# Kernel optimization log

Measured on AMD Instinct MI355X. Metric: run time of the kernel, lower is better.

## Reference

```python
import jax, jax.numpy as jnp
import numpy as np


def _grid_sample_bilinear_zeros(src, y, x):
    """Bilinear grid_sample, zeros padding, pixel-space coords.
    src: [B,C,H,W]; y,x: [B,H,W] float pixel coordinates (y along H, x along W).
    Returns [B,C,H,W].
    """
    B, C, H, W = src.shape
    y0 = jnp.floor(y)
    x0 = jnp.floor(x)
    y1 = y0 + 1.0
    x1 = x0 + 1.0
    wy1 = y - y0
    wy0 = 1.0 - wy1
    wx1 = x - x0
    wx0 = 1.0 - wx1

    b_idx = jnp.arange(B)[:, None, None]  # [B,1,1]

    def gather(yi, xi):
        valid = ((yi >= 0) & (yi < H) & (xi >= 0) & (xi < W)).astype(src.dtype)
        yc = jnp.clip(yi, 0, H - 1).astype(jnp.int32)
        xc = jnp.clip(xi, 0, W - 1).astype(jnp.int32)
        v = src[b_idx, :, yc, xc]  # advanced indexing -> [B,H,W,C]
        return v * valid[..., None]

    out = (gather(y0, x0) * (wy0 * wx0)[..., None]
           + gather(y0, x1) * (wy0 * wx1)[..., None]
           + gather(y1, x0) * (wy1 * wx0)[..., None]
           + gather(y1, x1) * (wy1 * wx1)[..., None])  # [B,H,W,C]
    return out.transpose(0, 3, 1, 2)


def setup_inputs() -> dict:
    key = jax.random.key(0)
    k1, k2 = jax.random.split(key)
    B, C, H, W = 8, 64, 256, 256
    src = jax.random.normal(k1, (B, C, H, W), dtype=jnp.float32)
    flow = jax.random.normal(k2, (B, 2, H, W), dtype=jnp.float32)
    return {"src": src, "flow": flow}


def reference(src, flow):
    B, C, H, W = src.shape
    # identity grid (meshgrid 'ij'): channel 0 = row index (H), channel 1 = col index (W)
    gy = jnp.arange(H, dtype=flow.dtype)[None, :, None]  # [1,H,1]
    gx = jnp.arange(W, dtype=flow.dtype)[None, None, :]  # [1,1,W]
    new_y = gy + flow[:, 0]  # [B,H,W]
    new_x = gx + flow[:, 1]
    # normalize to [-1,1] (as the module does) ...
    ny = 2.0 * (new_y / (H - 1) - 0.5)
    nx = 2.0 * (new_x / (W - 1) - 0.5)
    # ... then grid_sample with align_corners=True maps back to pixel space
    py = (ny + 1.0) * 0.5 * (H - 1)
    px = (nx + 1.0) * 0.5 * (W - 1)
    return _grid_sample_bilinear_zeros(src, py, px)
```

## Files before the change

### kernel.cpp

```cpp
#include <hip/hip_runtime.h>

#define B_ 8
#define C_ 64
#define H_ 256
#define W_ 256
#define RT 8
#define CG 8
#define WIN 32
#define PITCH 264

__global__ __launch_bounds__(256) void st_warp_kernel(
    const float* __restrict__ src,
    const float* __restrict__ flow,
    float* __restrict__ out)
{
    __shared__ float tile[WIN * PITCH];

    const int HW = H_ * W_;

    int id    = blockIdx.x;
    int b     = id & 7;
    int local = id >> 3;
    int rt    = local & 31;
    int cg    = local >> 5;
    int r0    = rt * RT;
    int cbase = cg * CG;
    int w     = threadIdx.x;

    int ylo = r0 - 12;
    ylo = ylo < 0 ? 0 : (ylo > H_ - WIN ? H_ - WIN : ylo);

    int   o0[RT], o1[RT];
    float a00[RT], a01[RT], a10[RT], a11[RT];
    unsigned m0 = 0, m1 = 0;

    const float* flow_b = flow + (size_t)b * 2 * HW;

    #pragma unroll
    for (int j = 0; j < RT; ++j) {
        int h = r0 + j;
        float fy = flow_b[h * W_ + w];
        float fx = flow_b[HW + h * W_ + w];
        float new_y = (float)h + fy;
        float new_x = (float)w + fx;
        float ny = 2.0f * (new_y / (float)(H_ - 1) - 0.5f);
        float nx = 2.0f * (new_x / (float)(W_ - 1) - 0.5f);
        float py = (ny + 1.0f) * 0.5f * (float)(H_ - 1);
        float px = (nx + 1.0f) * 0.5f * (float)(W_ - 1);

        float y0f = floorf(py), x0f = floorf(px);
        int y0 = (int)y0f, x0 = (int)x0f;
        int y1 = y0 + 1,  x1 = x0 + 1;
        float wy1 = py - y0f, wy0 = 1.0f - wy1;
        float wx1 = px - x0f, wx0 = 1.0f - wx1;

        bool vy0 = (y0 >= 0) & (y0 < H_);
        bool vy1 = (y1 >= 0) & (y1 < H_);
        bool vx0 = (x0 >= 0) & (x0 < W_);
        bool vx1 = (x1 >= 0) & (x1 < W_);

        a00[j] = wy0 * wx0 * (float)(vy0 & vx0);
        a01[j] = wy0 * wx1 * (float)(vy0 & vx1);
        a10[j] = wy1 * wx0 * (float)(vy1 & vx0);
        a11[j] = wy1 * wx1 * (float)(vy1 & vx1);

        int y0c = min(max(y0, 0), H_ - 1);
        int y1c = min(max(y1, 0), H_ - 1);
        int x0c = min(max(x0, 0), W_ - 1);
        int x1c = min(max(x1, 0), W_ - 1);

        int xl = min(max(x0, 0), W_ - 2);
        if (x0c != xl) m0 |= (1u << j);
        if (x1c == xl) m1 |= (1u << j);

        int rl0 = min(max(y0c - ylo, 0), WIN - 1);
        int rl1 = min(max(y1c - ylo, 0), WIN - 1);
        o0[j] = rl0 * PITCH + xl;
        o1[j] = rl1 * PITCH + xl;
    }

    int rowblk = threadIdx.x >> 6;
    int col    = (threadIdx.x & 63) * 4;

    size_t chan_stride = (size_t)HW;
    const float* sc0 = src + ((size_t)(b * C_ + cbase)) * chan_stride + (size_t)ylo * W_;
    float*       oc0 = out + ((size_t)(b * C_ + cbase)) * chan_stride + (size_t)r0 * W_ + w;

    for (int c = 0; c < CG; ++c) {
        const float* sc = sc0 + (size_t)c * chan_stride;
        float*       oc = oc0 + (size_t)c * chan_stride;

        #pragma unroll
        for (int it = 0; it < WIN / 4; ++it) {
            int r = it * 4 + rowblk;
            float4 v = *(const float4*)(sc + r * W_ + col);
            *(float4*)&tile[r * PITCH + col] = v;
        }
        __syncthreads();

        #pragma unroll
        for (int j = 0; j < RT; ++j) {
            float p0x = tile[o0[j]], p0y = tile[o0[j] + 1];
            float p1x = tile[o1[j]], p1y = tile[o1[j] + 1];
            float q00 = (m0 >> j) & 1 ? p0y : p0x;
            float q01 = (m1 >> j) & 1 ? p0x : p0y;
            float q10 = (m0 >> j) & 1 ? p1y : p1x;
            float q11 = (m1 >> j) & 1 ? p1x : p1y;
            float v = q00 * a00[j] + q01 * a01[j] + q10 * a10[j] + q11 * a11[j];
            __builtin_nontemporal_store(v, oc + j * W_);
        }
        __syncthreads();
    }
}

extern "C" void kernel_launch(void* const* d_in, const int* in_sizes, int n_in,
                              void* d_out, int out_size, void* d_ws, size_t ws_size,
                              hipStream_t stream) {
    const float* src  = (const float*)d_in[0];
    const float* flow = (const float*)d_in[1];
    float* out = (float*)d_out;
    dim3 grid(B_ * (H_ / RT) * (C_ / CG));
    dim3 block(256);
    st_warp_kernel<<<grid, block, 0, stream>>>(src, flow, out);
}
```

Baseline: 242.6 us.

## Double rows per block, load tile via direct global-to-LDS, fold corner selects into weights

Each block now handles 16 output rows instead of 8, which halves the block count and reuses each loaded 32-row source window across more outputs. Tile fills switch from float4 register round-trips to the global_load_lds builtin, which writes straight into shared memory. Per-row state is compressed: the x-edge select masks are folded into four precomputed weights, and the second row offset is rebuilt from a one-bit mask, to cut register pressure alongside the new launch_bounds occupancy hint. The risk is that flows pointing more than about 8 rows away get clamped into the window incorrectly, and that direct LDS loads with a padded pitch may not place data as intended.

```diff
diff --git a/kernel.cpp b/kernel.cpp
--- a/kernel.cpp
+++ b/kernel.cpp
@@ -4,12 +4,12 @@
 #define C_ 64
 #define H_ 256
 #define W_ 256
-#define RT 8
+#define RT 16
 #define CG 8
 #define WIN 32
 #define PITCH 264
 
-__global__ __launch_bounds__(256) void st_warp_kernel(
+__global__ __launch_bounds__(256, 4) void st_warp_kernel(
     const float* __restrict__ src,
     const float* __restrict__ flow,
     float* __restrict__ out)
@@ -21,18 +21,18 @@
     int id    = blockIdx.x;
     int b     = id & 7;
     int local = id >> 3;
-    int rt    = local & 31;
-    int cg    = local >> 5;
+    int rt    = local & 15;
+    int cg    = local >> 4;
     int r0    = rt * RT;
     int cbase = cg * CG;
     int w     = threadIdx.x;
 
-    int ylo = r0 - 12;
+    int ylo = r0 - 8;
     ylo = ylo < 0 ? 0 : (ylo > H_ - WIN ? H_ - WIN : ylo);
 
-    int   o0[RT], o1[RT];
-    float a00[RT], a01[RT], a10[RT], a11[RT];
-    unsigned m0 = 0, m1 = 0;
+    int   o0[RT];
+    float b00[RT], b01[RT], b10[RT], b11[RT];
+    unsigned md = 0;
 
     const float* flow_b = flow + (size_t)b * 2 * HW;
 
@@ -59,54 +59,57 @@
         bool vx0 = (x0 >= 0) & (x0 < W_);
         bool vx1 = (x1 >= 0) & (x1 < W_);
 
-        a00[j] = wy0 * wx0 * (float)(vy0 & vx0);
-        a01[j] = wy0 * wx1 * (float)(vy0 & vx1);
-        a10[j] = wy1 * wx0 * (float)(vy1 & vx0);
-        a11[j] = wy1 * wx1 * (float)(vy1 & vx1);
+        float a00 = wy0 * wx0 * (float)(vy0 & vx0);
+        float a01 = wy0 * wx1 * (float)(vy0 & vx1);
+        float a10 = wy1 * wx0 * (float)(vy1 & vx0);
+        float a11 = wy1 * wx1 * (float)(vy1 & vx1);
 
         int y0c = min(max(y0, 0), H_ - 1);
         int y1c = min(max(y1, 0), H_ - 1);
         int x0c = min(max(x0, 0), W_ - 1);
         int x1c = min(max(x1, 0), W_ - 1);
+        int xl  = min(max(x0, 0), W_ - 2);
 
-        int xl = min(max(x0, 0), W_ - 2);
-        if (x0c != xl) m0 |= (1u << j);
-        if (x1c == xl) m1 |= (1u << j);
+        bool s0 = (x0c == xl);
+        bool s1 = (x1c == xl);
+        b00[j] = (s0 ? a00 : 0.0f) + (s1 ? a01 : 0.0f);
+        b01[j] = (s0 ? 0.0f : a00) + (s1 ? 0.0f : a01);
+        b10[j] = (s0 ? a10 : 0.0f) + (s1 ? a11 : 0.0f);
+        b11[j] = (s0 ? 0.0f : a10) + (s1 ? 0.0f : a11);
 
         int rl0 = min(max(y0c - ylo, 0), WIN - 1);
         int rl1 = min(max(y1c - ylo, 0), WIN - 1);
         o0[j] = rl0 * PITCH + xl;
-        o1[j] = rl1 * PITCH + xl;
+        if (rl1 == rl0 + 1) md |= (1u << j);
     }
 
-    int rowblk = threadIdx.x >> 6;
-    int col    = (threadIdx.x & 63) * 4;
+    int wv   = threadIdx.x >> 6;
+    int lane = threadIdx.x & 63;
 
-    size_t chan_stride = (size_t)HW;
-    const float* sc0 = src + ((size_t)(b * C_ + cbase)) * chan_stride + (size_t)ylo * W_;
-    float*       oc0 = out + ((size_t)(b * C_ + cbase)) * chan_stride + (size_t)r0 * W_ + w;
+    const float* sc0 = src + ((size_t)(b * C_ + cbase)) * HW + (size_t)ylo * W_;
+    float*       oc0 = out + ((size_t)(b * C_ + cbase)) * HW + (size_t)r0 * W_ + w;
 
     for (int c = 0; c < CG; ++c) {
-        const float* sc = sc0 + (size_t)c * chan_stride;
-        float*       oc = oc0 + (size_t)c * chan_stride;
+        const float* sc = sc0 + (size_t)c * HW;
 
         #pragma unroll
         for (int it = 0; it < WIN / 4; ++it) {
-            int r = it * 4 + rowblk;
-            float4 v = *(const float4*)(sc + r * W_ + col);
-            *(float4*)&tile[r * PITCH + col] = v;
+            int r = it * 4 + wv;
+            __builtin_amdgcn_global_load_lds(
+                (const __attribute__((address_space(1))) void*)(sc + r * W_ + (lane << 2)),
+                (__attribute__((address_space(3))) void*)(&tile[r * PITCH]),
+                16, 0, 0);
         }
         __syncthreads();
 
+        float* oc = oc0 + (size_t)c * HW;
         #pragma unroll
         for (int j = 0; j < RT; ++j) {
-            float p0x = tile[o0[j]], p0y = tile[o0[j] + 1];
-            float p1x = tile[o1[j]], p1y = tile[o1[j] + 1];
-            float q00 = (m0 >> j) & 1 ? p0y : p0x;
-            float q01 = (m1 >> j) & 1 ? p0x : p0y;
-            float q10 = (m0 >> j) & 1 ? p1y : p1x;
-            float q11 = (m1 >> j) & 1 ? p1x : p1y;
-            float v = q00 * a00[j] + q01 * a01[j] + q10 * a10[j] + q11 * a11[j];
+            int off0 = o0[j];
+            float p0x = tile[off0], p0y = tile[off0 + 1];
+            int off1 = off0 + (((md >> j) & 1) ? PITCH : 0);
+            float p1x = tile[off1], p1y = tile[off1 + 1];
+            float v = p0x * b00[j] + p0y * b01[j] + p1x * b10[j] + p1y * b11[j];
             __builtin_nontemporal_store(v, oc + j * W_);
         }
         __syncthreads();
```

Measured after the change: 245.7 us. Within noise of the previous version (+1.3%).
